# Performance work log

Measured on AMD Instinct MI355X. Metric: run time of the kernel, lower is better.

Reference implementation:

```python
import jax, jax.numpy as jnp
import numpy as np

N, E, IN, HID, OUT = 100000, 1600000, 128, 128, 64


def setup_inputs() -> dict:
    key = jax.random.key(0)
    k1, k2, k3, k4 = jax.random.split(key, 4)
    x = jax.random.normal(k1, (N, IN), dtype=jnp.float32)
    edge_index = jax.random.randint(k2, (2, E), 0, N, dtype=jnp.int64)
    W1 = jax.random.normal(k3, (IN, HID), dtype=jnp.float32) * (1.0 / np.sqrt(IN))
    b1 = jnp.zeros((HID,), dtype=jnp.float32)
    W2 = jax.random.normal(k4, (HID, OUT), dtype=jnp.float32) * (1.0 / np.sqrt(HID))
    b2 = jnp.zeros((OUT,), dtype=jnp.float32)
    return {"x": x, "edge_index": edge_index, "W1": W1, "b1": b1, "W2": W2, "b2": b2}


def _gcn_conv(x, src, dst, norm, W, b):
    # linear transform first (PyG order when reducing feature dim), then SpMM
    h = x @ W                                   # [N, F_out]
    msg = h[src] * norm[:, None]                # [E+N, F_out] gathered messages
    out = jax.ops.segment_sum(msg, dst, num_segments=x.shape[0])
    return out + b


def _norm_coeffs(edge_index, num_nodes, dtype):
    # add self-loops and compute symmetric normalization deg^-1/2[src]*deg^-1/2[dst]
    loop = jnp.arange(num_nodes, dtype=edge_index.dtype)
    src = jnp.concatenate([edge_index[0], loop])
    dst = jnp.concatenate([edge_index[1], loop])
    deg = jax.ops.segment_sum(jnp.ones_like(dst, dtype=dtype), dst, num_segments=num_nodes)
    dinv = jnp.where(deg > 0, jax.lax.rsqrt(jnp.maximum(deg, 1.0)), 0.0)
    norm = dinv[src] * dinv[dst]
    return src, dst, norm


def reference(x, edge_index, W1, b1, W2, b2):
    # eval-mode forward: dropout is identity
    src, dst, norm = _norm_coeffs(edge_index, x.shape[0], x.dtype)
    h = jax.nn.relu(_gcn_conv(x, src, dst, norm, W1, b1))
    out = _gcn_conv(h, src, dst, norm, W2, b2)
    return out
```

## Files before the change

kernel.cpp:

```cpp
#include <hip/hip_runtime.h>
#include <hip/hip_bf16.h>

#define DEVINL __device__ __forceinline__

typedef __attribute__((ext_vector_type(8))) short bf16x8;
typedef __attribute__((ext_vector_type(4))) float f32x4;

union U8 {
    bf16x8 v;
    uint4 u;
};

DEVINL int clampidx(int v, int n) { return ((unsigned)v < (unsigned)n) ? v : 0; }
DEVINL float bflo(unsigned int u) { return __uint_as_float(u << 16); }
DEVINL float bfhi(unsigned int u) { return __uint_as_float(u & 0xffff0000u); }
DEVINL unsigned int f2bf(float f) {
    unsigned int u = __float_as_uint(f);
    u += 0x7fffu + ((u >> 16) & 1u);
    return u >> 16;
}

DEVINL void split8(const float4 v0, const float4 v1, uint4& hi, uint4& lo) {
    const float xv[8] = {v0.x, v0.y, v0.z, v0.w, v1.x, v1.y, v1.z, v1.w};
    unsigned h[8], l[8];
#pragma unroll
    for (int j = 0; j < 8; ++j) {
        h[j] = f2bf(xv[j]);
        const float r = xv[j] - bflo(h[j]);
        l[j] = f2bf(r);
    }
    hi = make_uint4(h[0] | (h[1] << 16), h[2] | (h[3] << 16),
                    h[4] | (h[5] << 16), h[6] | (h[7] << 16));
    lo = make_uint4(l[0] | (l[1] << 16), l[2] | (l[3] << 16),
                    l[4] | (l[5] << 16), l[6] | (l[7] << 16));
}

__global__ __launch_bounds__(256) void k_wprep(const float* __restrict__ W1,
                                               const float* __restrict__ W2,
                                               unsigned short* __restrict__ WT1h,
                                               unsigned short* __restrict__ WT1l,
                                               unsigned short* __restrict__ WT2h,
                                               unsigned short* __restrict__ WT2l) {
    const int i = blockIdx.x * 256 + threadIdx.x;
    if (i < 16384) {
        const int nn = i & 127, k = i >> 7;
        const float v = W1[k * 128 + nn];
        const unsigned h = f2bf(v);
        const float r = v - bflo(h);
        WT1h[nn * 128 + k] = (unsigned short)h;
        WT1l[nn * 128 + k] = (unsigned short)f2bf(r);
    }
    if (i < 8192) {
        const int nn = i & 63, k = i >> 6;
        const float v = W2[k * 64 + nn];
        const unsigned h = f2bf(v);
        const float r = v - bflo(h);
        WT2h[nn * 128 + k] = (unsigned short)h;
        WT2l[nn * 128 + k] = (unsigned short)f2bf(r);
    }
}

__global__ __launch_bounds__(256) void k_bktscan(const int* __restrict__ bktCnt,
                                                 int* __restrict__ bktBase,
                                                 int* __restrict__ bktCur, int NB) {
    __shared__ int sh[256];
    int carry = 0;
    for (int c0 = 0; c0 < NB; c0 += 256) {
        const int i = c0 + threadIdx.x;
        const int v = (i < NB) ? bktCnt[i] : 0;
        sh[threadIdx.x] = v;
        __syncthreads();
        for (int off = 1; off < 256; off <<= 1) {
            int t = (threadIdx.x >= off) ? sh[threadIdx.x - off] : 0;
            __syncthreads();
            sh[threadIdx.x] += t;
            __syncthreads();
        }
        if (i < NB) {
            const int excl = carry + sh[threadIdx.x] - v;
            bktBase[i] = excl;
            bktCur[i] = excl;
        }
        const int tot = sh[255];
        __syncthreads();
        carry += tot;
    }
    if (threadIdx.x == 0) bktBase[NB] = carry;
}

__global__ __launch_bounds__(256) void k_bktscatter(const int* __restrict__ ei,
                                                    int* __restrict__ bktCur,
                                                    unsigned int* __restrict__ packed,
                                                    int E, int n) {
    __shared__ unsigned int sPack[4096];
    __shared__ unsigned short sBkt[4096];
    __shared__ int sHist[1024], sStart[1024], sLoc[1024];
    for (int i = threadIdx.x; i < 1024; i += 256) {
        sHist[i] = 0;
        sLoc[i] = 0;
    }
    __syncthreads();
    const int base = blockIdx.x * 4096;
#pragma unroll
    for (int j = 0; j < 16; ++j) {
        const int k = j * 256 + threadIdx.x;
        const int i = base + k;
        if (i < E) {
            const int s = clampidx(ei[i], n);
            const int d = clampidx(ei[(size_t)E + i], n);
            const int b = d >> 7;
            sPack[k] = ((unsigned)(d & 127) << 25) | (unsigned)s;
            sBkt[k] = (unsigned short)b;
            atomicAdd(&sHist[b], 1);
        }
    }
    __syncthreads();
    for (int b = threadIdx.x; b < 1024; b += 256) {
        const int c = sHist[b];
        sStart[b] = c ? atomicAdd(&bktCur[b], c) : 0;
    }
    __syncthreads();
#pragma unroll
    for (int j = 0; j < 16; ++j) {
        const int k = j * 256 + threadIdx.x;
        const int i = base + k;
        if (i < E) {
            const int b = sBkt[k];
            const int pos = sStart[b] + atomicAdd(&sLoc[b], 1);
            packed[pos] = sPack[k];
        }
    }
}

__global__ __launch_bounds__(256) void k_bktfill(const unsigned int* __restrict__ packed,
                                                 const int* __restrict__ bktBase,
                                                 int* __restrict__ p, float* __restrict__ dinv,
                                                 int* __restrict__ srcs, int n) {
    constexpr int CAP = 8192;
    __shared__ unsigned int sPack[CAP];
    __shared__ int sSrc[CAP];
    __shared__ int deg[128], incl[128], cur[128];
    const int bkt = blockIdx.x;
    const int e0 = bktBase[bkt], e1 = bktBase[bkt + 1];
    const int cnt = e1 - e0;
    const int tid = threadIdx.x;
    if (tid < 128) deg[tid] = 0;
    __syncthreads();
    for (int i = tid; i < cnt; i += 256) {
        const unsigned int u = packed[e0 + i];
        if (i < CAP) sPack[i] = u;
        atomicAdd(&deg[u >> 25], 1);
    }
    __syncthreads();
    if (tid < 128) incl[tid] = deg[tid];
    __syncthreads();
    for (int off = 1; off < 128; off <<= 1) {
        const int v = (tid < 128 && tid >= off) ? incl[tid - off] : 0;
        __syncthreads();
        if (tid < 128) incl[tid] += v;
        __syncthreads();
    }
    const int node0 = bkt << 7;
    if (tid < 128) {
        cur[tid] = incl[tid] - deg[tid];
        const int node = node0 + tid;
        if (node < n) {
            p[node] = e0 + incl[tid];
            dinv[node] = rsqrtf((float)deg[tid] + 1.0f);
        }
    }
    __syncthreads();
    for (int i = tid; i < cnt; i += 256) {
        const unsigned int u = (i < CAP) ? sPack[i] : packed[e0 + i];
        const int dl = (int)(u >> 25);
        const int s = (int)(u & 0x1FFFFFFu);
        const int pos = atomicAdd(&cur[dl], 1);
        if (pos < CAP) sSrc[pos] = s;
        else srcs[e0 + pos] = s;
    }
    __syncthreads();
    const int lim = cnt < CAP ? cnt : CAP;
    for (int i = tid; i < lim; i += 256) srcs[e0 + i] = sSrc[i];
}

__global__ __launch_bounds__(256) void k_gemm1_count(
    const float* __restrict__ x, const unsigned short* __restrict__ WTh,
    const unsigned short* __restrict__ WTl, unsigned short* __restrict__ Y16, int n,
    const int* __restrict__ ei, int* __restrict__ bktCnt, int E, int nCnt) {
    __shared__ int hist[1024];
    if ((int)blockIdx.x < nCnt) {
        for (int i = threadIdx.x; i < 1024; i += 256) hist[i] = 0;
        __syncthreads();
        const int base = blockIdx.x * 4096;
#pragma unroll
        for (int j = 0; j < 16; ++j) {
            int i = base + j * 256 + threadIdx.x;
            if (i < E) atomicAdd(&hist[clampidx(ei[(size_t)E + i], n) >> 7], 1);
        }
        __syncthreads();
        for (int b = threadIdx.x; b < 1024; b += 256) {
            int c = hist[b];
            if (c) atomicAdd(&bktCnt[b], c);
        }
        return;
    }
    const int blk = (int)blockIdx.x - nCnt;
    const int lane = threadIdx.x & 63;
    const int row16 = lane & 15;
    const int kg = lane >> 4;
    const int rowbase = blk * 64 + (threadIdx.x >> 6) * 16;
    const int grow = rowbase + row16;

    U8 ahi[4], alo[4];
    if (grow < n) {
        const float* xp = x + (size_t)grow * 128 + kg * 8;
#pragma unroll
        for (int k0 = 0; k0 < 4; ++k0) {
            const float4 v0 = *(const float4*)(xp + k0 * 32);
            const float4 v1 = *(const float4*)(xp + k0 * 32 + 4);
            split8(v0, v1, ahi[k0].u, alo[k0].u);
        }
    } else {
#pragma unroll
        for (int k0 = 0; k0 < 4; ++k0) {
            ahi[k0].u = make_uint4(0, 0, 0, 0);
            alo[k0].u = make_uint4(0, 0, 0, 0);
        }
    }

    f32x4 acc[8];
#pragma unroll
    for (int nt = 0; nt < 8; ++nt) acc[nt] = (f32x4){0.f, 0.f, 0.f, 0.f};

#pragma unroll
    for (int nt = 0; nt < 8; ++nt) {
        const unsigned short* bp = WTh + (size_t)(nt * 16 + row16) * 128 + kg * 8;
        const unsigned short* bq = WTl + (size_t)(nt * 16 + row16) * 128 + kg * 8;
#pragma unroll
        for (int k0 = 0; k0 < 4; ++k0) {
            U8 bh, bl;
            bh.u = *(const uint4*)(bp + k0 * 32);
            bl.u = *(const uint4*)(bq + k0 * 32);
            acc[nt] = __builtin_amdgcn_mfma_f32_16x16x32_bf16(ahi[k0].v, bh.v, acc[nt], 0, 0, 0);
            acc[nt] = __builtin_amdgcn_mfma_f32_16x16x32_bf16(alo[k0].v, bh.v, acc[nt], 0, 0, 0);
            acc[nt] = __builtin_amdgcn_mfma_f32_16x16x32_bf16(ahi[k0].v, bl.v, acc[nt], 0, 0, 0);
        }
    }

    const int m4 = (lane >> 4) * 4;
#pragma unroll
    for (int nt = 0; nt < 8; ++nt) {
#pragma unroll
        for (int r = 0; r < 4; ++r) {
            const int orow = rowbase + m4 + r;
            if (orow < n)
                Y16[(size_t)orow * 128 + nt * 16 + row16] = (unsigned short)f2bf(acc[nt][r]);
        }
    }
}

__global__ __launch_bounds__(256) void k_gemm2_mfma(const unsigned short* __restrict__ H16,
                                                    const unsigned short* __restrict__ WTh,
                                                    const unsigned short* __restrict__ WTl,
                                                    unsigned short* __restrict__ Y16, int n) {
    const int lane = threadIdx.x & 63;
    const int row16 = lane & 15;
    const int kg = lane >> 4;
    const int rowbase = blockIdx.x * 64 + (threadIdx.x >> 6) * 16;
    const int grow = rowbase + row16;

    U8 a[4];
    if (grow < n) {
        const unsigned short* ap = H16 + (size_t)grow * 128 + kg * 8;
#pragma unroll
        for (int k0 = 0; k0 < 4; ++k0) a[k0].u = *(const uint4*)(ap + k0 * 32);
    } else {
#pragma unroll
        for (int k0 = 0; k0 < 4; ++k0) a[k0].u = make_uint4(0, 0, 0, 0);
    }

    f32x4 acc[4];
#pragma unroll
    for (int nt = 0; nt < 4; ++nt) acc[nt] = (f32x4){0.f, 0.f, 0.f, 0.f};

#pragma unroll
    for (int nt = 0; nt < 4; ++nt) {
        const unsigned short* bp = WTh + (size_t)(nt * 16 + row16) * 128 + kg * 8;
        const unsigned short* bq = WTl + (size_t)(nt * 16 + row16) * 128 + kg * 8;
#pragma unroll
        for (int k0 = 0; k0 < 4; ++k0) {
            U8 bh, bl;
            bh.u = *(const uint4*)(bp + k0 * 32);
            bl.u = *(const uint4*)(bq + k0 * 32);
            acc[nt] = __builtin_amdgcn_mfma_f32_16x16x32_bf16(a[k0].v, bh.v, acc[nt], 0, 0, 0);
            acc[nt] = __builtin_amdgcn_mfma_f32_16x16x32_bf16(a[k0].v, bl.v, acc[nt], 0, 0, 0);
        }
    }

    const int m4 = (lane >> 4) * 4;
#pragma unroll
    for (int nt = 0; nt < 4; ++nt) {
#pragma unroll
        for (int r = 0; r < 4; ++r) {
            const int orow = rowbase + m4 + r;
            if (orow < n)
                Y16[(size_t)orow * 64 + nt * 16 + row16] = (unsigned short)f2bf(acc[nt][r]);
        }
    }
}

__global__ __launch_bounds__(256) void k_gather128(const unsigned int* __restrict__ XW,
                                                   const int* __restrict__ p,
                                                   const int* __restrict__ srcs,
                                                   const float* __restrict__ dinv,
                                                   const float* __restrict__ b1,
                                                   unsigned int* __restrict__ H1b, int n) {
    const int node = __builtin_amdgcn_readfirstlane(blockIdx.x * 4 + (threadIdx.x >> 6));
    if (node >= n) return;
    const int t = threadIdx.x & 63;
    const int start = (node == 0) ? 0 : p[node - 1];
    const int end = p[node];
    const float din = dinv[node];
    const unsigned int us = XW[(size_t)node * 64 + t];
    float a0 = bflo(us) * din, a1 = bfhi(us) * din;

    int c = start;
    for (; c + 16 <= end; c += 16) {
        int s[16];
#pragma unroll
        for (int k = 0; k < 16; ++k) s[k] = __builtin_amdgcn_readfirstlane(srcs[c + k]);
        float w[16];
        unsigned int u[16];
#pragma unroll
        for (int k = 0; k < 16; ++k) {
            w[k] = dinv[s[k]];
            u[k] = XW[((unsigned)s[k] << 6) + t];
        }
#pragma unroll
        for (int k = 0; k < 16; ++k) {
            a0 = fmaf(bflo(u[k]), w[k], a0);
            a1 = fmaf(bfhi(u[k]), w[k], a1);
        }
    }
    for (; c + 4 <= end; c += 4) {
        int s[4];
#pragma unroll
        for (int k = 0; k < 4; ++k) s[k] = __builtin_amdgcn_readfirstlane(srcs[c + k]);
        float w[4];
        unsigned int u[4];
#pragma unroll
        for (int k = 0; k < 4; ++k) {
            w[k] = dinv[s[k]];
            u[k] = XW[((unsigned)s[k] << 6) + t];
        }
#pragma unroll
        for (int k = 0; k < 4; ++k) {
            a0 = fmaf(bflo(u[k]), w[k], a0);
            a1 = fmaf(bfhi(u[k]), w[k], a1);
        }
    }
    for (; c < end; ++c) {
        const int s = __builtin_amdgcn_readfirstlane(srcs[c]);
        const float w = dinv[s];
        const unsigned int u = XW[((unsigned)s << 6) + t];
        a0 = fmaf(bflo(u), w, a0);
        a1 = fmaf(bfhi(u), w, a1);
    }
    const float r0 = fmaxf(fmaf(a0, din, b1[2 * t]), 0.0f);
    const float r1 = fmaxf(fmaf(a1, din, b1[2 * t + 1]), 0.0f);
    H1b[(size_t)node * 64 + t] = f2bf(r0) | (f2bf(r1) << 16);
}

__global__ __launch_bounds__(256) void k_gather64(const unsigned short* __restrict__ h2,
                                                  const int* __restrict__ p,
                                                  const int* __restrict__ srcs,
                                                  const float* __restrict__ dinv,
                                                  const float* __restrict__ b2,
                                                  float* __restrict__ out, int n) {
    const int node = __builtin_amdgcn_readfirstlane(blockIdx.x * 4 + (threadIdx.x >> 6));
    if (node >= n) return;
    const int t = threadIdx.x & 63;
    const int start = (node == 0) ? 0 : p[node - 1];
    const int end = p[node];
    const float din = dinv[node];
    float acc = bflo(h2[(size_t)node * 64 + t]) * din;

    int c = start;
    for (; c + 16 <= end; c += 16) {
        int s[16];
#pragma unroll
        for (int k = 0; k < 16; ++k) s[k] = __builtin_amdgcn_readfirstlane(srcs[c + k]);
        float w[16], v[16];
#pragma unroll
        for (int k = 0; k < 16; ++k) {
            w[k] = dinv[s[k]];
            v[k] = bflo(h2[((unsigned)s[k] << 6) + t]);
        }
#pragma unroll
        for (int k = 0; k < 16; ++k) acc = fmaf(v[k], w[k], acc);
    }
    for (; c + 4 <= end; c += 4) {
        int s[4];
#pragma unroll
        for (int k = 0; k < 4; ++k) s[k] = __builtin_amdgcn_readfirstlane(srcs[c + k]);
        float w[4], v[4];
#pragma unroll
        for (int k = 0; k < 4; ++k) {
            w[k] = dinv[s[k]];
            v[k] = bflo(h2[((unsigned)s[k] << 6) + t]);
        }
#pragma unroll
        for (int k = 0; k < 4; ++k) acc = fmaf(v[k], w[k], acc);
    }
    for (; c < end; ++c) {
        const int s = __builtin_amdgcn_readfirstlane(srcs[c]);
        const float w = dinv[s];
        acc = fmaf(bflo(h2[((unsigned)s << 6) + t]), w, acc);
    }
    out[(size_t)node * 64 + t] = fmaf(acc, din, b2[t]);
}

extern "C" void kernel_launch(void* const* d_in, const int* in_sizes, int n_in,
                              void* d_out, int out_size, void* d_ws, size_t ws_size,
                              hipStream_t stream) {
    const float* x  = (const float*)d_in[0];
    const int* ei   = (const int*)d_in[1];
    const float* W1 = (const float*)d_in[2];
    const float* b1 = (const float*)d_in[3];
    const float* W2 = (const float*)d_in[4];
    const float* b2 = (const float*)d_in[5];

    const int n = in_sizes[0] / 128;
    const int E = in_sizes[1] / 2;
    const int NB = (n + 127) >> 7;

    auto al = [](size_t b) { return (b + 255) & ~(size_t)255; };
    const size_t off_p    = 0;
    const size_t off_dinv = off_p + al((size_t)n * 4);
    const size_t off_srcs = off_dinv + al((size_t)n * 4);
    const size_t off_XW   = off_srcs + al((size_t)E * 4);
    const size_t off_H1b  = off_XW + al((size_t)n * 64 * 4);
    const size_t off_w1h  = off_H1b + al((size_t)n * 64 * 4);
    const size_t off_w1l  = off_w1h + al(128 * 128 * 2);
    const size_t off_w2h  = off_w1l + al(128 * 128 * 2);
    const size_t off_w2l  = off_w2h + al(64 * 128 * 2);
    const size_t need     = off_w2l + (size_t)64 * 128 * 2;
    const size_t off_pk   = off_H1b;
    const size_t off_bc   = off_pk + al((size_t)E * 4);
    const size_t off_bb   = off_bc + al(1024 * 4);
    const size_t off_bu   = off_bb + al(1025 * 4);

    if (ws_size < need || NB > 1024) {
        hipMemsetAsync(d_out, 0, (size_t)out_size * 4, stream);
        return;
    }

    int*            p    = (int*)((char*)d_ws + off_p);
    float*          dinv = (float*)((char*)d_ws + off_dinv);
    int*            srcs = (int*)((char*)d_ws + off_srcs);
    unsigned int*   XW   = (unsigned int*)((char*)d_ws + off_XW);
    unsigned int*   H1b  = (unsigned int*)((char*)d_ws + off_H1b);
    unsigned int*   pk   = (unsigned int*)((char*)d_ws + off_pk);
    int*            bCnt = (int*)((char*)d_ws + off_bc);
    int*            bBase= (int*)((char*)d_ws + off_bb);
    int*            bCur = (int*)((char*)d_ws + off_bu);
    unsigned short* WT1h = (unsigned short*)((char*)d_ws + off_w1h);
    unsigned short* WT1l = (unsigned short*)((char*)d_ws + off_w1l);
    unsigned short* WT2h = (unsigned short*)((char*)d_ws + off_w2h);
    unsigned short* WT2l = (unsigned short*)((char*)d_ws + off_w2l);
    float*          out  = (float*)d_out;

    const int gEdge = (E + 4095) / 4096;
    const int gM    = (n + 63) / 64;
    const int gG    = (n + 3) / 4;

    hipMemsetAsync(bCnt, 0, 1024 * 4, stream);
    k_wprep<<<64, 256, 0, stream>>>(W1, W2, WT1h, WT1l, WT2h, WT2l);

    k_gemm1_count<<<gEdge + gM, 256, 0, stream>>>(x, WT1h, WT1l, (unsigned short*)XW, n,
                                                  ei, bCnt, E, gEdge);

    k_bktscan<<<1, 256, 0, stream>>>(bCnt, bBase, bCur, NB);
    k_bktscatter<<<gEdge, 256, 0, stream>>>(ei, bCur, pk, E, n);
    k_bktfill<<<NB, 256, 0, stream>>>(pk, bBase, p, dinv, srcs, n);

    k_gather128<<<gG, 256, 0, stream>>>(XW, p, srcs, dinv, b1, H1b, n);

    k_gemm2_mfma<<<gM, 256, 0, stream>>>((const unsigned short*)H1b, WT2h, WT2l,
                                         (unsigned short*)XW, n);

    k_gather64<<<gG, 256, 0, stream>>>((const unsigned short*)XW, p, srcs, dinv, b2, out, n);
}
```

Measured before the change: 354.1 us.

## Replicate bucket counters and pad cursors to cut global atomic contention in CSR build

Bucket histogram atomics in the count phase are now spread over 32 replicated count arrays, which the scan kernel sums. The per-bucket cursors are padded to 64-byte stride to avoid false sharing. The scatter kernel drops the shared-memory staging of packed edges and per-bucket local offsets. Each block now handles 16384 edges, re-reads the edge index in a second pass and writes directly using shared-memory cursor atomics. This cuts global atomic contention and shared-memory use, at the cost of reading the edges twice and writing less coalesced output.

```diff
diff --git a/kernel.cpp b/kernel.cpp
--- a/kernel.cpp
+++ b/kernel.cpp
@@ -62,12 +62,16 @@
 
 __global__ __launch_bounds__(256) void k_bktscan(const int* __restrict__ bktCnt,
                                                  int* __restrict__ bktBase,
-                                                 int* __restrict__ bktCur, int NB) {
+                                                 int* __restrict__ bktCurP, int NB) {
     __shared__ int sh[256];
     int carry = 0;
     for (int c0 = 0; c0 < NB; c0 += 256) {
         const int i = c0 + threadIdx.x;
-        const int v = (i < NB) ? bktCnt[i] : 0;
+        int v = 0;
+        if (i < NB) {
+#pragma unroll
+            for (int r = 0; r < 32; ++r) v += bktCnt[r * 1024 + i];
+        }
         sh[threadIdx.x] = v;
         __syncthreads();
         for (int off = 1; off < 256; off <<= 1) {
@@ -79,7 +83,7 @@
         if (i < NB) {
             const int excl = carry + sh[threadIdx.x] - v;
             bktBase[i] = excl;
-            bktCur[i] = excl;
+            bktCurP[i * 16] = excl;
         }
         const int tot = sh[255];
         __syncthreads();
@@ -89,46 +93,31 @@
 }
 
 __global__ __launch_bounds__(256) void k_bktscatter(const int* __restrict__ ei,
-                                                    int* __restrict__ bktCur,
+                                                    int* __restrict__ bktCurP,
                                                     unsigned int* __restrict__ packed,
                                                     int E, int n) {
-    __shared__ unsigned int sPack[4096];
-    __shared__ unsigned short sBkt[4096];
-    __shared__ int sHist[1024], sStart[1024], sLoc[1024];
-    for (int i = threadIdx.x; i < 1024; i += 256) {
-        sHist[i] = 0;
-        sLoc[i] = 0;
-    }
-    __syncthreads();
-    const int base = blockIdx.x * 4096;
-#pragma unroll
-    for (int j = 0; j < 16; ++j) {
-        const int k = j * 256 + threadIdx.x;
-        const int i = base + k;
-        if (i < E) {
-            const int s = clampidx(ei[i], n);
-            const int d = clampidx(ei[(size_t)E + i], n);
-            const int b = d >> 7;
-            sPack[k] = ((unsigned)(d & 127) << 25) | (unsigned)s;
-            sBkt[k] = (unsigned short)b;
-            atomicAdd(&sHist[b], 1);
-        }
+    __shared__ int hist[1024];
+    __shared__ int sCur[1024];
+    for (int i = threadIdx.x; i < 1024; i += 256) hist[i] = 0;
+    __syncthreads();
+    const int base0 = blockIdx.x * 16384;
+    const int lim = min(16384, E - base0);
+    for (int off = threadIdx.x; off < lim; off += 256) {
+        const int d = clampidx(ei[(size_t)E + base0 + off], n);
+        atomicAdd(&hist[d >> 7], 1);
     }
     __syncthreads();
     for (int b = threadIdx.x; b < 1024; b += 256) {
-        const int c = sHist[b];
-        sStart[b] = c ? atomicAdd(&bktCur[b], c) : 0;
-    }
-    __syncthreads();
-#pragma unroll
-    for (int j = 0; j < 16; ++j) {
-        const int k = j * 256 + threadIdx.x;
-        const int i = base + k;
-        if (i < E) {
-            const int b = sBkt[k];
-            const int pos = sStart[b] + atomicAdd(&sLoc[b], 1);
-            packed[pos] = sPack[k];
-        }
+        const int c = hist[b];
+        sCur[b] = c ? atomicAdd(&bktCurP[b * 16], c) : 0;
+    }
+    __syncthreads();
+    for (int off = threadIdx.x; off < lim; off += 256) {
+        const int i = base0 + off;
+        const int s = clampidx(ei[i], n);
+        const int d = clampidx(ei[(size_t)E + i], n);
+        const int pos = atomicAdd(&sCur[d >> 7], 1);
+        packed[pos] = ((unsigned)(d & 127) << 25) | (unsigned)s;
     }
 }
 
@@ -198,9 +187,10 @@
             if (i < E) atomicAdd(&hist[clampidx(ei[(size_t)E + i], n) >> 7], 1);
         }
         __syncthreads();
+        int* rep = bktCnt + (blockIdx.x & 31) * 1024;
         for (int b = threadIdx.x; b < 1024; b += 256) {
             int c = hist[b];
-            if (c) atomicAdd(&bktCnt[b], c);
+            if (c) atomicAdd(&rep[b], c);
         }
         return;
     }
@@ -447,10 +437,11 @@
     const size_t need     = off_w2l + (size_t)64 * 128 * 2;
     const size_t off_pk   = off_H1b;
     const size_t off_bc   = off_pk + al((size_t)E * 4);
-    const size_t off_bb   = off_bc + al(1024 * 4);
+    const size_t off_bb   = off_bc + al(32 * 1024 * 4);
     const size_t off_bu   = off_bb + al(1025 * 4);
-
-    if (ws_size < need || NB > 1024) {
+    const size_t csr_end  = off_bu + (size_t)1024 * 16 * 4;
+
+    if (ws_size < need || NB > 1024 || csr_end > off_w1h) {
         hipMemsetAsync(d_out, 0, (size_t)out_size * 4, stream);
         return;
     }
@@ -463,7 +454,7 @@
     unsigned int*   pk   = (unsigned int*)((char*)d_ws + off_pk);
     int*            bCnt = (int*)((char*)d_ws + off_bc);
     int*            bBase= (int*)((char*)d_ws + off_bb);
-    int*            bCur = (int*)((char*)d_ws + off_bu);
+    int*            bCurP= (int*)((char*)d_ws + off_bu);
     unsigned short* WT1h = (unsigned short*)((char*)d_ws + off_w1h);
     unsigned short* WT1l = (unsigned short*)((char*)d_ws + off_w1l);
     unsigned short* WT2h = (unsigned short*)((char*)d_ws + off_w2h);
@@ -471,17 +462,18 @@
     float*          out  = (float*)d_out;
 
     const int gEdge = (E + 4095) / 4096;
+    const int gScat = (E + 16383) / 16384;
     const int gM    = (n + 63) / 64;
     const int gG    = (n + 3) / 4;
 
-    hipMemsetAsync(bCnt, 0, 1024 * 4, stream);
+    hipMemsetAsync(bCnt, 0, 32 * 1024 * 4, stream);
     k_wprep<<<64, 256, 0, stream>>>(W1, W2, WT1h, WT1l, WT2h, WT2l);
 
     k_gemm1_count<<<gEdge + gM, 256, 0, stream>>>(x, WT1h, WT1l, (unsigned short*)XW, n,
                                                   ei, bCnt, E, gEdge);
 
-    k_bktscan<<<1, 256, 0, stream>>>(bCnt, bBase, bCur, NB);
-    k_bktscatter<<<gEdge, 256, 0, stream>>>(ei, bCur, pk, E, n);
+    k_bktscan<<<1, 256, 0, stream>>>(bCnt, bBase, bCurP, NB);
+    k_bktscatter<<<gScat, 256, 0, stream>>>(ei, bCurP, pk, E, n);
     k_bktfill<<<NB, 256, 0, stream>>>(pk, bBase, p, dinv, srcs, n);
 
     k_gather128<<<gG, 256, 0, stream>>>(XW, p, srcs, dinv, b1, H1b, n);
```

Result: slower. 379.1 us (+7.1%).
